# Kernel optimization log

Hardware: AMD Instinct MI355X
Metric: run time of the kernel (lower is better)

## Reference

```python
import jax, jax.numpy as jnp
import numpy as np

B, C, H, W = 8, 256, 128, 128
M = C // 8  # query/key reduced channels (scale=8)
EPS = 1e-6


def setup_inputs() -> dict:
    key = jax.random.key(0)
    ks = jax.random.split(key, 9)
    s = 0.02
    return {
        "x": jax.random.normal(ks[0], (B, C, H, W), jnp.float32),
        "wq": jax.random.normal(ks[1], (M, C), jnp.float32) * s,
        "bq": jax.random.normal(ks[2], (M,), jnp.float32) * s,
        "wk": jax.random.normal(ks[3], (M, C), jnp.float32) * s,
        "bk": jax.random.normal(ks[4], (M,), jnp.float32) * s,
        "wv": jax.random.normal(ks[5], (C, C), jnp.float32) * s,
        "bv": jax.random.normal(ks[6], (C,), jnp.float32) * s,
        "gamma_k": jax.random.normal(ks[7], (1,), jnp.float32) * 0.1,
        "gamma_c": jax.random.normal(ks[8], (1,), jnp.float32) * 0.1,
    }


def _conv1x1(x, w, b):
    # 1x1 conv == per-pixel linear map over channels
    return jnp.einsum("oc,bchw->bohw", w, x) + b[None, :, None, None]


def reference(x, wq, bq, wk, bk, wv, bv, gamma_k, gamma_c):
    b, c, h, w = x.shape
    n = h * w

    # ---- KernelAttentionModule (softplus linear attention, O(n)) ----
    Q = jax.nn.softplus(_conv1x1(x, wq, bq)).reshape(b, -1, n).transpose(0, 2, 1)  # [b,n,m]
    K = jax.nn.softplus(_conv1x1(x, wk, bk)).reshape(b, -1, n)                      # [b,m,n]
    V = _conv1x1(x, wv, bv).reshape(b, c, n)                                        # [b,c,n]
    KV = jnp.einsum("bmn,bcn->bmc", K, V)                                           # [b,m,c]
    norm = 1.0 / jnp.einsum("bnm,bm->bn", Q, jnp.sum(K, axis=-1) + EPS)             # [b,n]
    weight_value = jnp.einsum("bnm,bmc,bn->bcn", Q, KV, norm).reshape(b, c, h, w)
    kam = x + gamma_k * weight_value

    # ---- ChannelAttentionModule (channel bmm attention) ----
    pq = x.reshape(b, c, n)
    energy = jnp.einsum("bcn,bdn->bcd", pq, pq)                                     # [b,c,c]
    energy_new = jnp.max(energy, axis=-1, keepdims=True) - energy
    attn = jax.nn.softmax(energy_new, axis=-1)
    cam = gamma_c * jnp.einsum("bcd,bdn->bcn", attn, pq).reshape(b, c, h, w)

    return kam + cam
```

## Files before the change

### kernel.cpp

```cpp
#include <hip/hip_runtime.h>
#include <math.h>

#define NPIX 16384
#define CH 256
#define MDIM 32
#define NB 8
#define EPSF 1e-6f
#define SPLIT 16
#define KCH (NPIX / SPLIT)

#define XKPART_F32OFF 16777216ull

#define GRAM_BLKS 384
#define KX_BLKS   2048

typedef short short4v __attribute__((ext_vector_type(4)));
typedef short short8 __attribute__((ext_vector_type(8)));
typedef _Float16 half8 __attribute__((ext_vector_type(8)));
typedef float f32x4 __attribute__((ext_vector_type(4)));

__device__ inline unsigned short f2h(float v) {
    return __builtin_bit_cast(unsigned short, (_Float16)v);
}
__device__ inline float h2f(unsigned short h) {
    return (float)__builtin_bit_cast(_Float16, h);
}

__global__ void k_prep(const float* __restrict__ wq, const float* __restrict__ wk,
                       unsigned short* __restrict__ WQB, unsigned short* __restrict__ WKB)
{
    int i = blockIdx.x * 256 + threadIdx.x;
    WQB[i] = f2h(wq[i]);
    WKB[i] = f2h(wk[i]);
}

__global__ __launch_bounds__(256, 4) void k_work1(
    const float* __restrict__ x,
    const unsigned short* __restrict__ WKB, const unsigned short* __restrict__ WQB,
    const float* __restrict__ bk, const float* __restrict__ bq,
    unsigned short* __restrict__ xkpart, float* __restrict__ Ksum,
    unsigned short* __restrict__ Qg, float* __restrict__ enpart)
{
    __shared__ unsigned short ldsbuf[20480];
    const int bid = blockIdx.x;
    const int tid = threadIdx.x;

    if (bid < GRAM_BLKS) {
        unsigned short* As = ldsbuf;
        unsigned short* Bs = ldsbuf + 9216;
        const int tile = bid % 3;
        const int rest = bid / 3;
        const int sp = rest & 15, b = rest >> 4;
        const int rt = (tile == 2) ? 1 : 0;
        const int ct = (tile == 0) ? 0 : 1;
        const bool diag = (rt == ct);
        const int r0 = rt * 128, c0 = ct * 128;
        const float* xb = x + (size_t)b * CH * NPIX;
        const int k0base = sp * KCH;

        unsigned short* Bs_p = diag ? As : Bs;

        const int wave = tid >> 6, lane = tid & 63;
        const int wr = wave >> 1, wc = wave & 1;

        f32x4 acc[4][4];
        #pragma unroll
        for (int i = 0; i < 4; ++i)
            #pragma unroll
            for (int j = 0; j < 4; ++j)
                acc[i][j] = (f32x4){0.f, 0.f, 0.f, 0.f};

        const int oct = tid & 7;
        const int frow = tid >> 3;

        for (int kk = 0; kk < KCH; kk += 64) {
            __syncthreads();
            const int k0 = k0base + kk;
            #pragma unroll
            for (int half = 0; half < 2; ++half) {
                if (half && diag) continue;
                const int rowbase = half ? c0 : r0;
                unsigned short* Hs = half ? Bs : As;
                #pragma unroll
                for (int s = 0; s < 4; ++s) {
                    const int r = frow + s * 32;
                    const float* src = xb + (size_t)(rowbase + r) * NPIX + k0 + oct * 8;
                    float4 v0 = *(const float4*)src;
                    float4 v1 = *(const float4*)(src + 4);
                    float vv[8] = {v0.x, v0.y, v0.z, v0.w, v1.x, v1.y, v1.z, v1.w};
                    short8 p;
                    #pragma unroll
                    for (int e = 0; e < 8; ++e) p[e] = (short)f2h(vv[e]);
                    *(short8*)&Hs[r * 72 + oct * 8] = p;
                }
            }
            __syncthreads();

            #pragma unroll
            for (int ks2 = 0; ks2 < 2; ++ks2) {
                short8 a4[4], b4[4];
                const int rbase = wr * 64 + (lane & 15);
                const int cbase = wc * 64 + (lane & 15);
                const int koff = ks2 * 32 + (lane >> 4) * 8;
                #pragma unroll
                for (int f = 0; f < 4; ++f) {
                    a4[f] = *(const short8*)&As[(rbase + f * 16) * 72 + koff];
                    b4[f] = *(const short8*)&Bs_p[(cbase + f * 16) * 72 + koff];
                }
                #pragma unroll
                for (int i = 0; i < 4; ++i)
                    #pragma unroll
                    for (int j = 0; j < 4; ++j)
                        acc[i][j] = __builtin_amdgcn_mfma_f32_16x16x32_f16(
                            __builtin_bit_cast(half8, a4[i]),
                            __builtin_bit_cast(half8, b4[j]), acc[i][j], 0, 0, 0);
            }
        }

        float* ep = enpart + (size_t)(sp * NB + b) * (CH * CH);
        const int rw = (lane >> 4) * 4;
        const int cw = lane & 15;
        #pragma unroll
        for (int i = 0; i < 4; ++i)
            #pragma unroll
            for (int j = 0; j < 4; ++j) {
                const int row = r0 + wr * 64 + i * 16 + rw;
                const int col = c0 + wc * 64 + j * 16 + cw;
                #pragma unroll
                for (int q = 0; q < 4; ++q) {
                    float v = acc[i][j][q];
                    ep[(size_t)(row + q) * CH + col] = v;
                    if (!diag) ep[(size_t)col * CH + (row + q)] = v;
                }
            }
    } else {
        unsigned short* xs  = ldsbuf;
        unsigned short* ksm = ldsbuf + 18432;
        const int u = bid - GRAM_BLKS;
        const int b = u >> 8, t = u & 255;
        const int n0 = t * 64;
        const int w = tid >> 6, l = tid & 63;
        const int li = l & 15, lg = l >> 4;
        const float* xb = x + (size_t)b * CH * NPIX;

        #pragma unroll
        for (int s = 0; s < 8; ++s) {
            int e8 = tid + s * 256;
            int c = e8 >> 3, j8 = e8 & 7;
            const float* src = xb + (size_t)c * NPIX + n0 + j8 * 8;
            float4 v0 = *(const float4*)src;
            float4 v1 = *(const float4*)(src + 4);
            float vv[8] = {v0.x, v0.y, v0.z, v0.w, v1.x, v1.y, v1.z, v1.w};
            short8 p;
            #pragma unroll
            for (int e = 0; e < 8; ++e) p[e] = (short)f2h(vv[e]);
            const int g = j8 ^ (c & 7) ^ ((c >> 3) & 7);
            *(short8*)&xs[c * 72 + g * 8] = p;
        }
        __syncthreads();

        {
            f32x4 accK[2], accQ[2];
            #pragma unroll
            for (int i = 0; i < 2; ++i) {
                accK[i] = (f32x4){0.f, 0.f, 0.f, 0.f};
                accQ[i] = (f32x4){0.f, 0.f, 0.f, 0.f};
            }
            const int n = w * 16 + li;
            const int gn = n >> 3, inn = n & 7;
            #pragma unroll
            for (int kc = 0; kc < 8; ++kc) {
                short8 bxw;
                #pragma unroll
                for (int e = 0; e < 8; ++e) {
                    const int d = kc * 32 + lg * 8 + e;
                    const int g = gn ^ e ^ ((kc * 4 + lg) & 7);
                    bxw[e] = (short)xs[d * 72 + g * 8 + inn];
                }
                half8 bx = __builtin_bit_cast(half8, bxw);
                #pragma unroll
                for (int i = 0; i < 2; ++i) {
                    const size_t wo = (size_t)(i * 16 + li) * CH + kc * 32 + lg * 8;
                    half8 kw = __builtin_bit_cast(half8, *(const short8*)(WKB + wo));
                    half8 qw = __builtin_bit_cast(half8, *(const short8*)(WQB + wo));
                    accK[i] = __builtin_amdgcn_mfma_f32_16x16x32_f16(kw, bx, accK[i], 0, 0, 0);
                    accQ[i] = __builtin_amdgcn_mfma_f32_16x16x32_f16(qw, bx, accQ[i], 0, 0, 0);
                }
            }
            unsigned short* qp = Qg + ((size_t)b * NPIX + n0 + n) * MDIM;
            #pragma unroll
            for (int i = 0; i < 2; ++i) {
                short4v q4;
                #pragma unroll
                for (int q = 0; q < 4; ++q) {
                    const int m = i * 16 + lg * 4 + q;
                    float kv = accK[i][q] + bk[m];
                    kv = fmaxf(kv, 0.f) + log1pf(expf(-fabsf(kv)));
                    ksm[m * 64 + (n ^ ((m & 7) << 3))] = f2h(kv);
                    float qv = accQ[i][q] + bq[m];
                    qv = fmaxf(qv, 0.f) + log1pf(expf(-fabsf(qv)));
                    q4[q] = (short)f2h(qv);
                }
                *(short4v*)(qp + i * 16 + lg * 4) = q4;
            }
        }
        __syncthreads();

        if (tid < MDIM) {
            float s = 0.f;
            #pragma unroll
            for (int j = 0; j < 64; ++j)
                s += h2f(ksm[tid * 64 + (j ^ ((tid & 7) << 3))]);
            atomicAdd(&Ksum[b * MDIM + tid], s);
        }

        f32x4 axk[4][2];
        #pragma unroll
        for (int i = 0; i < 4; ++i)
            #pragma unroll
            for (int j = 0; j < 2; ++j) axk[i][j] = (f32x4){0.f, 0.f, 0.f, 0.f};

        #pragma unroll
        for (int ks2 = 0; ks2 < 2; ++ks2) {
            const int nc = ks2 * 32 + lg * 8;
            half8 kfr[2];
            #pragma unroll
            for (int j = 0; j < 2; ++j) {
                const int m = j * 16 + li;
                kfr[j] = __builtin_bit_cast(half8,
                    *(const short8*)&ksm[m * 64 + (nc ^ ((m & 7) << 3))]);
            }
            #pragma unroll
            for (int i = 0; i < 4; ++i) {
                const int d = w * 64 + i * 16 + li;
                const int g = (nc >> 3) ^ (d & 7) ^ ((d >> 3) & 7);
                half8 xf = __builtin_bit_cast(half8, *(const short8*)&xs[d * 72 + g * 8]);
                #pragma unroll
                for (int j = 0; j < 2; ++j)
                    axk[i][j] = __builtin_amdgcn_mfma_f32_16x16x32_f16(xf, kfr[j], axk[i][j], 0, 0, 0);
            }
        }

        unsigned short* xkp = xkpart + (size_t)(b * 256 + t) * MDIM * CH;
        #pragma unroll
        for (int i = 0; i < 4; ++i)
            #pragma unroll
            for (int j = 0; j < 2; ++j) {
                short4v pk;
                #pragma unroll
                for (int q = 0; q < 4; ++q) pk[q] = (short)f2h(axk[i][j][q]);
                *(short4v*)(xkp + (size_t)(j * 16 + li) * CH + w * 64 + i * 16 + lg * 4) = pk;
            }
    }
}

__global__ void k_work2(const unsigned short* __restrict__ xkpart,
                        float* __restrict__ XKR,
                        const float* __restrict__ enpart,
                        const float* __restrict__ gc,
                        unsigned short* __restrict__ attnb)
{
    __shared__ float red[8];
    const int bid = blockIdx.x;
    if (bid < 1024) {
        const int bx = bid & 255;
        const int b = bx >> 5, m = bx & 31, d = threadIdx.x;
        const int t0 = (bid >> 8) * 64;
        float s = 0.f;
        #pragma unroll 4
        for (int t = t0; t < t0 + 64; ++t)
            s += h2f(xkpart[(((size_t)b * 256 + t) * MDIM + m) * CH + d]);
        atomicAdd(&XKR[((size_t)b * MDIM + m) * CH + d], s);
    } else {
        const int bid2 = bid - 1024;
        const int b = bid2 >> 8, c = bid2 & 255;
        const int d = threadIdx.x;
        float e = 0.f;
        #pragma unroll
        for (int sp = 0; sp < SPLIT; ++sp)
            e += enpart[(size_t)(sp * NB + b) * (CH * CH) + (size_t)c * CH + d];
        float mn = e;
        #pragma unroll
        for (int o = 1; o < 64; o <<= 1) mn = fminf(mn, __shfl_xor(mn, o));
        if ((d & 63) == 0) red[d >> 6] = mn;
        __syncthreads();
        mn = fminf(fminf(red[0], red[1]), fminf(red[2], red[3]));
        float w = expf(mn - e);
        float s = w;
        #pragma unroll
        for (int o = 1; o < 64; o <<= 1) s += __shfl_xor(s, o);
        if ((d & 63) == 0) red[4 + (d >> 6)] = s;
        __syncthreads();
        s = red[4] + red[5] + red[6] + red[7];
        attnb[((size_t)(b * CH) + c) * CH + d] = f2h(gc[0] * w / s);
    }
}

__global__ void k_kv(const float* __restrict__ wv, const float* __restrict__ bv,
                     const float* __restrict__ XKR, const float* __restrict__ Ksum,
                     unsigned short* __restrict__ KVTb) {
    const int b = blockIdx.x, q = blockIdx.y;
    const int ci = threadIdx.x & 63, mg = threadIdx.x >> 6;
    const int c = q * 64 + ci;
    float s[8];
    const float bvc = bv[c];
    #pragma unroll
    for (int i = 0; i < 8; ++i) s[i] = bvc * Ksum[b * MDIM + mg * 8 + i];
    #pragma unroll 4
    for (int d = 0; d < CH; ++d) {
        float w = wv[(size_t)c * CH + d];
        #pragma unroll
        for (int i = 0; i < 8; ++i)
            s[i] = fmaf(w, XKR[((size_t)b * MDIM + mg * 8 + i) * CH + d], s[i]);
    }
    short8 p;
    #pragma unroll
    for (int i = 0; i < 8; ++i) p[i] = (short)f2h(s[i]);
    *(short8*)(KVTb + ((size_t)b * CH + c) * MDIM + mg * 8) = p;
}

__global__ __launch_bounds__(256, 4) void k_final(
    const float* __restrict__ x, const unsigned short* __restrict__ Qg,
    const unsigned short* __restrict__ KVTb, const float* __restrict__ Ksum,
    const unsigned short* __restrict__ attnb, const float* __restrict__ gk,
    float* __restrict__ out)
{
    __shared__ uint2 xsTv[4096];
    unsigned char* xsT = (unsigned char*)xsTv;
    const int b = blockIdx.y, n0 = blockIdx.x * 64, tid = threadIdx.x;
    const int w = tid >> 6, l = tid & 63;
    const int li = l & 15, lg = l >> 4;
    const float* xb = x + (size_t)b * CH * NPIX;

    short8 qb[4];
    #pragma unroll
    for (int j = 0; j < 4; ++j)
        qb[j] = *(const short8*)(Qg +
            ((size_t)b * NPIX + n0 + j * 16 + li) * MDIM + lg * 8);
    float4 ks0 = *(const float4*)(Ksum + b * MDIM + lg * 8);
    float4 ks1 = *(const float4*)(Ksum + b * MDIM + lg * 8 + 4);
    const float kse[8] = {ks0.x + EPSF, ks0.y + EPSF, ks0.z + EPSF, ks0.w + EPSF,
                          ks1.x + EPSF, ks1.y + EPSF, ks1.z + EPSF, ks1.w + EPSF};

    {
        const int n4 = li * 4;
        const bool o1 = lg & 1, o2 = (lg >> 1) & 1;
        #pragma unroll 4
        for (int p = 0; p < 16; ++p) {
            const int d0 = w * 64 + p * 4;
            float4 vv = *(const float4*)(xb + (size_t)(d0 + lg) * NPIX + n0 + n4);
            float v0 = vv.x, v1 = vv.y, v2 = vv.z, v3 = vv.w;
            float r1 = __shfl_xor(o1 ? v0 : v1, 16);
            float r2 = __shfl_xor(o1 ? v2 : v3, 16);
            float a0 = o1 ? r1 : v0, a1 = o1 ? v1 : r1;
            float a2 = o1 ? r2 : v2, a3 = o1 ? v3 : r2;
            float r3 = __shfl_xor(o2 ? a0 : a2, 32);
            float r4 = __shfl_xor(o2 ? a1 : a3, 32);
            float b0 = o2 ? r3 : a0, b1 = o2 ? r4 : a1;
            float b2 = o2 ? a2 : r3, b3 = o2 ? a3 : r4;
            const int nl = n4 + lg;
            unsigned lo = (unsigned)f2h(b0) | ((unsigned)f2h(b1) << 16);
            unsigned hi = (unsigned)f2h(b2) | ((unsigned)f2h(b3) << 16);
            const int off = nl * 512 +
                ((2 * d0) ^ ((nl & 7) << 4) ^ (((nl >> 3) & 1) << 3));
            *(uint2*)(xsT + off) = make_uint2(lo, hi);
        }
    }

    f32x4 acc[4][4];
    #pragma unroll
    for (int i = 0; i < 4; ++i)
        #pragma unroll
        for (int j = 0; j < 4; ++j)
            acc[i][j] = (f32x4){0.f, 0.f, 0.f, 0.f};

    {
        const float gkv = gk[0];
        half8 qs[4];
        #pragma unroll
        for (int j = 0; j < 4; ++j) {
            float qf[8];
            float den = 0.f;
            #pragma unroll
            for (int e = 0; e < 8; ++e) {
                qf[e] = h2f((unsigned short)qb[j][e]);
                den = fmaf(qf[e], kse[e], den);
            }
            den += __shfl_xor(den, 16);
            den += __shfl_xor(den, 32);
            const float nrm = gkv / den;
            #pragma unroll
            for (int e = 0; e < 8; ++e) qs[j][e] = (_Float16)(qf[e] * nrm);
        }
        #pragma unroll
        for (int i = 0; i < 4; ++i) {
            half8 ka = __builtin_bit_cast(half8, *(const short8*)(KVTb +
                ((size_t)b * CH + w * 64 + i * 16 + li) * MDIM + lg * 8));
            #pragma unroll
            for (int j = 0; j < 4; ++j)
                acc[i][j] = __builtin_amdgcn_mfma_f32_16x16x32_f16(qs[j], ka, acc[i][j], 0, 0, 0);
        }
    }
    __syncthreads();

    const unsigned short* ab = attnb + (size_t)b * CH * CH;
    for (int kk = 0; kk < CH; kk += 32) {
        half8 bx[4];
        #pragma unroll
        for (int j = 0; j < 4; ++j) {
            const int nf = j * 16 + li;
            const int d2 = 2 * (kk + lg * 8);
            const int sw = ((nf & 7) << 4) ^ (((nf >> 3) & 1) << 3);
            uint2 h0 = *(const uint2*)(xsT + nf * 512 + (d2 ^ sw));
            uint2 h1 = *(const uint2*)(xsT + nf * 512 + ((d2 + 8) ^ sw));
            int4 tmp = make_int4(h0.x, h0.y, h1.x, h1.y);
            bx[j] = __builtin_bit_cast(half8, tmp);
        }
        #pragma unroll
        for (int i = 0; i < 4; ++i) {
            half8 af = __builtin_bit_cast(half8, *(const short8*)(ab +
                (size_t)(w * 64 + i * 16 + li) * CH + kk + lg * 8));
            #pragma unroll
            for (int j = 0; j < 4; ++j)
                acc[i][j] = __builtin_amdgcn_mfma_f32_16x16x32_f16(bx[j], af, acc[i][j], 0, 0, 0);
        }
    }

    float* outb = out + (size_t)b * CH * NPIX;
    #pragma unroll
    for (int i = 0; i < 4; ++i) {
        const int c = w * 64 + i * 16 + li;
        #pragma unroll
        for (int j = 0; j < 4; ++j) {
            const size_t idx = (size_t)c * NPIX + n0 + j * 16 + lg * 4;
            float4 xv = *(const float4*)(xb + idx);
            float4 v = make_float4(xv.x + acc[i][j][0], xv.y + acc[i][j][1],
                                   xv.z + acc[i][j][2], xv.w + acc[i][j][3]);
            *(float4*)(outb + idx) = v;
        }
    }
}

extern "C" void kernel_launch(void* const* d_in, const int* in_sizes, int n_in,
                              void* d_out, int out_size, void* d_ws, size_t ws_size,
                              hipStream_t stream)
{
    const float* x  = (const float*)d_in[0];
    const float* wq = (const float*)d_in[1];
    const float* bq = (const float*)d_in[2];
    const float* wk = (const float*)d_in[3];
    const float* bk = (const float*)d_in[4];
    const float* wv = (const float*)d_in[5];
    const float* bv = (const float*)d_in[6];
    const float* gk = (const float*)d_in[7];
    const float* gc = (const float*)d_in[8];
    float* out = (float*)d_out;
    char* wsb = (char*)d_ws;

    unsigned short* ATTB = (unsigned short*)(wsb);
    unsigned short* KVTB = (unsigned short*)(wsb + 1048576);
    float* KSUM = (float*)(wsb + 1179648);
    float* XKR  = (float*)(wsb + 1180672);
    unsigned short* WQB = (unsigned short*)(wsb + 1442816);
    unsigned short* WKB = (unsigned short*)(wsb + 1459200);
    unsigned short* QG  = (unsigned short*)(wsb + 1508352);

    unsigned short* xkpart = (unsigned short*)out;
    float* enpart = out + XKPART_F32OFF;

    hipMemsetAsync(KSUM, 0, 1024 + 262144, stream);

    k_prep<<<dim3(32), dim3(256), 0, stream>>>(wq, wk, WQB, WKB);
    k_work1<<<dim3(GRAM_BLKS + KX_BLKS), dim3(256), 0, stream>>>(
        x, WKB, WQB, bk, bq, xkpart, KSUM, QG, enpart);
    k_work2<<<dim3(3072), dim3(256), 0, stream>>>(xkpart, XKR, enpart, gc, ATTB);
    k_kv<<<dim3(NB, 4), dim3(256), 0, stream>>>(wv, bv, XKR, KSUM, KVTB);
    k_final<<<dim3(NPIX / 64, NB), dim3(256), 0, stream>>>(x, QG, KVTB, KSUM,
                                                           ATTB, gk, out);
}
```

Baseline: 227.5 us.

## Use MFMA for KV projection and remap Gram blocks across XCDs

The KV kernel drops its scalar FMA loop over 256 channels and uses fp16 16x16x32 MFMA instructions, converting wv and XKR to half on the fly. It now runs 8 blocks, one per batch, with each wave covering 64 output channels. Separately, Gram block indices are remapped so that the three tiles of the same (batch, split) pair land on the same XCD for L2 reuse of x. The MFMA path adds fp16 rounding of inputs and uses fewer blocks, which could lower parallelism for this small kernel.

```diff
diff --git a/kernel.cpp b/kernel.cpp
--- a/kernel.cpp
+++ b/kernel.cpp
@@ -48,9 +48,10 @@
     if (bid < GRAM_BLKS) {
         unsigned short* As = ldsbuf;
         unsigned short* Bs = ldsbuf + 9216;
-        const int tile = bid % 3;
-        const int rest = bid / 3;
-        const int sp = rest & 15, b = rest >> 4;
+        const int xcd = bid & 7, slot = bid >> 3;
+        const int grp = xcd * 16 + slot / 3;
+        const int tile = slot % 3;
+        const int sp = grp & 15, b = grp >> 4;
         const int rt = (tile == 2) ? 1 : 0;
         const int ct = (tile == 0) ? 0 : 1;
         const bool diag = (rt == ct);
@@ -299,24 +300,59 @@
 __global__ void k_kv(const float* __restrict__ wv, const float* __restrict__ bv,
                      const float* __restrict__ XKR, const float* __restrict__ Ksum,
                      unsigned short* __restrict__ KVTb) {
-    const int b = blockIdx.x, q = blockIdx.y;
-    const int ci = threadIdx.x & 63, mg = threadIdx.x >> 6;
-    const int c = q * 64 + ci;
-    float s[8];
-    const float bvc = bv[c];
+    const int b = blockIdx.x, tid = threadIdx.x;
+    const int w = tid >> 6, l = tid & 63;
+    const int li = l & 15, lg = l >> 4;
+
+    f32x4 acc[4][2];
     #pragma unroll
-    for (int i = 0; i < 8; ++i) s[i] = bvc * Ksum[b * MDIM + mg * 8 + i];
-    #pragma unroll 4
-    for (int d = 0; d < CH; ++d) {
-        float w = wv[(size_t)c * CH + d];
-        #pragma unroll
-        for (int i = 0; i < 8; ++i)
-            s[i] = fmaf(w, XKR[((size_t)b * MDIM + mg * 8 + i) * CH + d], s[i]);
-    }
-    short8 p;
+    for (int i = 0; i < 4; ++i)
+        #pragma unroll
+        for (int j = 0; j < 2; ++j) acc[i][j] = (f32x4){0.f, 0.f, 0.f, 0.f};
+
+    for (int kk = 0; kk < CH; kk += 32) {
+        half8 bfr[2];
+        #pragma unroll
+        for (int j = 0; j < 2; ++j) {
+            const int m = j * 16 + li;
+            const float* sp = XKR + ((size_t)b * MDIM + m) * CH + kk + lg * 8;
+            float4 v0 = *(const float4*)sp;
+            float4 v1 = *(const float4*)(sp + 4);
+            bfr[j][0] = (_Float16)v0.x; bfr[j][1] = (_Float16)v0.y;
+            bfr[j][2] = (_Float16)v0.z; bfr[j][3] = (_Float16)v0.w;
+            bfr[j][4] = (_Float16)v1.x; bfr[j][5] = (_Float16)v1.y;
+            bfr[j][6] = (_Float16)v1.z; bfr[j][7] = (_Float16)v1.w;
+        }
+        #pragma unroll
+        for (int i = 0; i < 4; ++i) {
+            const int c = w * 64 + i * 16 + li;
+            const float* wp = wv + (size_t)c * CH + kk + lg * 8;
+            float4 w0 = *(const float4*)wp;
+            float4 w1 = *(const float4*)(wp + 4);
+            half8 afr;
+            afr[0] = (_Float16)w0.x; afr[1] = (_Float16)w0.y;
+            afr[2] = (_Float16)w0.z; afr[3] = (_Float16)w0.w;
+            afr[4] = (_Float16)w1.x; afr[5] = (_Float16)w1.y;
+            afr[6] = (_Float16)w1.z; afr[7] = (_Float16)w1.w;
+            #pragma unroll
+            for (int j = 0; j < 2; ++j)
+                acc[i][j] = __builtin_amdgcn_mfma_f32_16x16x32_f16(afr, bfr[j], acc[i][j], 0, 0, 0);
+        }
+    }
+
     #pragma unroll
-    for (int i = 0; i < 8; ++i) p[i] = (short)f2h(s[i]);
-    *(short8*)(KVTb + ((size_t)b * CH + c) * MDIM + mg * 8) = p;
+    for (int i = 0; i < 4; ++i)
+        #pragma unroll
+        for (int j = 0; j < 2; ++j) {
+            const int m = j * 16 + li;
+            const float ks = Ksum[b * MDIM + m];
+            #pragma unroll
+            for (int q = 0; q < 4; ++q) {
+                const int c = w * 64 + i * 16 + lg * 4 + q;
+                KVTb[((size_t)b * CH + c) * MDIM + m] =
+                    f2h(acc[i][j][q] + bv[c] * ks);
+            }
+        }
 }
 
 __global__ __launch_bounds__(256, 4) void k_final(
@@ -474,7 +510,7 @@
     k_work1<<<dim3(GRAM_BLKS + KX_BLKS), dim3(256), 0, stream>>>(
         x, WKB, WQB, bk, bq, xkpart, KSUM, QG, enpart);
     k_work2<<<dim3(3072), dim3(256), 0, stream>>>(xkpart, XKR, enpart, gc, ATTB);
-    k_kv<<<dim3(NB, 4), dim3(256), 0, stream>>>(wv, bv, XKR, KSUM, KVTB);
+    k_kv<<<dim3(NB), dim3(256), 0, stream>>>(wv, bv, XKR, KSUM, KVTB);
     k_final<<<dim3(NPIX / 64, NB), dim3(256), 0, stream>>>(x, QG, KVTB, KSUM,
                                                            ATTB, gk, out);
 }
```

Result: faster. 221.0 us (median of 3 runs) (-2.9%).
